# Performance work log

Hardware: AMD Instinct MI355X
Metric: run time of the kernel (lower is better)

The kernel has to match this reference:

```python
import jax, jax.numpy as jnp
import numpy as np

EPS = 1e-5
C1 = 64


def conv2d(x, w, pad):
    return jax.lax.conv_general_dilated(x, w, (1, 1), [(pad, pad), (pad, pad)],
                                        dimension_numbers=('NCHW', 'OIHW', 'NCHW'))


def batchnorm(x, scale, bias, mean, var):
    # inference-mode BN with running stats
    inv = scale * jax.lax.rsqrt(var + EPS)
    return x * inv[None, :, None, None] + (bias - mean * inv)[None, :, None, None]


def _interp_mat(n_out, n_in):
    # 1-D bilinear interpolation matrix, align_corners=True
    pos = jnp.linspace(0.0, n_in - 1.0, n_out)
    i0 = jnp.clip(jnp.floor(pos).astype(jnp.int32), 0, n_in - 1)
    i1 = jnp.clip(i0 + 1, 0, n_in - 1)
    w1 = pos - i0.astype(pos.dtype)
    r = jnp.arange(n_out)
    M = jnp.zeros((n_out, n_in), jnp.float32)
    M = M.at[r, i0].add(1.0 - w1).at[r, i1].add(w1)
    return M


def resize_ac(x, oh, ow):
    # bilinear resize with align_corners=True (matches F.interpolate/UpsamplingBilinear2d)
    Mh = _interp_mat(oh, x.shape[2])
    Mw = _interp_mat(ow, x.shape[3])
    return jnp.einsum('pw,nchw,oh->ncop', Mw, x, Mh)


def grid_sample_bilinear(img, grid):
    # img [N,C,H,W]; grid [N,Ho,Wo,2] (x,y) in [-1,1]; align_corners=False, zeros padding
    N, C, H, W = img.shape
    x = (grid[..., 0] + 1.0) * (W * 0.5) - 0.5
    y = (grid[..., 1] + 1.0) * (H * 0.5) - 0.5
    x0 = jnp.floor(x)
    y0 = jnp.floor(y)
    x1 = x0 + 1.0
    y1 = y0 + 1.0
    wx1 = x - x0
    wy1 = y - y0

    def gather(im, yi, xi):
        # im [C,H,W]; yi,xi [Ho,Wo] float pixel coords
        valid = (xi >= 0) & (xi <= W - 1) & (yi >= 0) & (yi <= H - 1)
        xc = jnp.clip(xi, 0, W - 1).astype(jnp.int32)
        yc = jnp.clip(yi, 0, H - 1).astype(jnp.int32)
        return im[:, yc, xc] * valid[None].astype(im.dtype)

    def sample_one(im, x0, x1, y0, y1, wx1, wy1):
        return (gather(im, y0, x0) * ((1 - wy1) * (1 - wx1))[None]
                + gather(im, y0, x1) * ((1 - wy1) * wx1)[None]
                + gather(im, y1, x0) * (wy1 * (1 - wx1))[None]
                + gather(im, y1, x1) * (wy1 * wx1)[None])

    return jax.vmap(sample_one)(img, x0, x1, y0, y1, wx1, wy1)


def warp(inp, out_h, out_w, delta):
    # build base grid exactly like bilinear_interpolate_torch_gridsample
    N, C, H, W = inp.shape
    ys = jnp.linspace(-1.0, 1.0, out_h)
    xs = jnp.linspace(-1.0, 1.0, out_w)
    gx = jnp.broadcast_to(xs[None, :], (out_h, out_w))
    gy = jnp.broadcast_to(ys[:, None], (out_h, out_w))
    base = jnp.stack([gx, gy], axis=-1)[None]  # [1,Ho,Wo,2]
    norm = jnp.array([W, H], inp.dtype)  # delta[...,0]/W, delta[...,1]/H
    grid = base + jnp.transpose(delta, (0, 2, 3, 1)) / norm
    return grid_sample_bilinear(inp, grid)


def forward(low_stage, high_stage, in_map,
            dg1_w1, dg1_scale, dg1_bias, dg1_mean, dg1_var, dg1_w2,
            dg2_w1, dg2_scale, dg2_bias, dg2_mean, dg2_var, dg2_w2,
            gamma, out_w, out_b):
    h, w = low_stage.shape[2], low_stage.shape[3]
    high = resize_ac(high_stage, h, w)
    imap = jax.nn.sigmoid(resize_ac(in_map, in_map.shape[2] * 2, in_map.shape[3] * 2))
    cat = jnp.concatenate([low_stage, high], axis=1)  # [N,2*C1,h,w]
    d1 = conv2d(batchnorm(conv2d(cat, dg1_w1, 0), dg1_scale, dg1_bias, dg1_mean, dg1_var), dg1_w2, 1)
    d2 = conv2d(batchnorm(conv2d(cat, dg2_w1, 0), dg2_scale, dg2_bias, dg2_mean, dg2_var), dg2_w2, 1)
    hi = warp(high, h, w, d1)
    lo = warp(low_stage, h, w, d2)
    hs = hi + lo
    f = gamma * hs * imap + hs
    o = conv2d(f, out_w, 1) + out_b[None, :, None, None]
    return f, o


def setup_inputs() -> dict:
    key = jax.random.key(0)
    ks = jax.random.split(key, 24)
    N, H, W = 8, 160, 160
    d = {}
    d['low_stage'] = jax.random.normal(ks[0], (N, C1, H, W), jnp.float32)
    d['high_stage'] = jax.random.normal(ks[1], (N, C1, H // 2, W // 2), jnp.float32)
    d['in_map'] = jax.random.normal(ks[2], (N, 1, H // 2, W // 2), jnp.float32)

    def bnp(k):
        k1, k2, k3, k4 = jax.random.split(k, 4)
        return (jax.random.normal(k1, (C1,)) * 0.1 + 1.0,
                jax.random.normal(k2, (C1,)) * 0.1,
                jax.random.normal(k3, (C1,)) * 0.1,
                jax.random.uniform(k4, (C1,), minval=0.5, maxval=1.5))

    for i, p in ((3, 'dg1'), (10, 'dg2')):
        d[p + '_w1'] = jax.random.normal(ks[i], (C1, 2 * C1, 1, 1), jnp.float32) * 0.05
        s, b, m, v = bnp(ks[i + 1])
        d[p + '_scale'], d[p + '_bias'], d[p + '_mean'], d[p + '_var'] = s, b, m, v
        d[p + '_w2'] = jax.random.normal(ks[i + 2], (2, C1, 3, 3), jnp.float32) * 0.05
    d['gamma'] = jnp.ones((1,), jnp.float32)
    d['out_w'] = jax.random.normal(ks[20], (1, C1, 3, 3), jnp.float32) * 0.05
    d['out_b'] = jnp.zeros((1,), jnp.float32)
    return d


def reference(low_stage, high_stage, in_map,
              dg1_w1, dg1_scale, dg1_bias, dg1_mean, dg1_var, dg1_w2,
              dg2_w1, dg2_scale, dg2_bias, dg2_mean, dg2_var, dg2_w2,
              gamma, out_w, out_b):
    return forward(low_stage, high_stage, in_map,
                   dg1_w1, dg1_scale, dg1_bias, dg1_mean, dg1_var, dg1_w2,
                   dg2_w1, dg2_scale, dg2_bias, dg2_mean, dg2_var, dg2_w2,
                   gamma, out_w, out_b)
```

## Files before the change

kernel.cpp:

```cpp
#include <hip/hip_runtime.h>
#include <cmath>

#define N_   8
#define C_   64
#define H_   160
#define W_   160
#define HW_  25600
#define HH_  80
#define WH_  80
#define FSZ_ (N_ * C_ * HW_)
#define PSZ_ (N_ * HW_)

typedef unsigned short ushort8v __attribute__((ext_vector_type(8)));
typedef short          bf16x8  __attribute__((ext_vector_type(8)));
typedef float          f32x4   __attribute__((ext_vector_type(4)));

__device__ __forceinline__ float bf2f(unsigned short u) {
    return __uint_as_float(((unsigned)u) << 16);
}
__device__ __forceinline__ unsigned short f2bf(float f) {
    unsigned u = __float_as_uint(f);
    u += 0x7FFF + ((u >> 16) & 1);
    return (unsigned short)(u >> 16);
}

__device__ __forceinline__ void gs_setup(float bgx, float bgy, float dx, float dy,
                                         int* idx, float* wgt)
{
    float px = ((bgx + dx * (1.f / 160.f)) + 1.f) * 80.f - 0.5f;
    float py = ((bgy + dy * (1.f / 160.f)) + 1.f) * 80.f - 0.5f;
    float x0f = floorf(px), y0f = floorf(py);
    float wx1 = px - x0f, wy1 = py - y0f, wx0 = 1.f - wx1, wy0 = 1.f - wy1;
    int x0 = (int)x0f, y0 = (int)y0f;
    float mx0 = ((unsigned)x0       < (unsigned)W_) ? 1.f : 0.f;
    float mx1 = ((unsigned)(x0 + 1) < (unsigned)W_) ? 1.f : 0.f;
    float my0 = ((unsigned)y0       < (unsigned)H_) ? 1.f : 0.f;
    float my1 = ((unsigned)(y0 + 1) < (unsigned)H_) ? 1.f : 0.f;
    int x0c = min(max(x0, 0), W_ - 1), x1c = min(max(x0 + 1, 0), W_ - 1);
    int y0c = min(max(y0, 0), H_ - 1), y1c = min(max(y0 + 1, 0), H_ - 1);
    idx[0] = y0c * W_ + x0c; wgt[0] = wy0 * wx0 * my0 * mx0;
    idx[1] = y0c * W_ + x1c; wgt[1] = wy0 * wx1 * my0 * mx1;
    idx[2] = y1c * W_ + x0c; wgt[2] = wy1 * wx0 * my1 * mx0;
    idx[3] = y1c * W_ + x1c; wgt[3] = wy1 * wx1 * my1 * mx1;
}

__global__ __launch_bounds__(128) void compose_w_kernel(
    const float* __restrict__ w1a, const float* __restrict__ w1b,
    const float* __restrict__ s1, const float* __restrict__ b1,
    const float* __restrict__ m1, const float* __restrict__ v1,
    const float* __restrict__ s2, const float* __restrict__ b2,
    const float* __restrict__ m2, const float* __restrict__ v2,
    const float* __restrict__ w2a, const float* __restrict__ w2b,
    float* __restrict__ weffg, float* __restrict__ btap4)
{
    __shared__ float ws2[64], bpart[64];
    int bId = blockIdx.x;
    int row = bId / 9, tap = bId % 9;
    int br = row >> 1, oc = row & 1;
    int tid = threadIdx.x;

    const float* w1 = br ? w1b : w1a;
    const float* w2 = br ? w2b : w2a;

    if (tid < 64) {
        int mid = tid;
        float sc = br ? s2[mid] : s1[mid];
        float vv = br ? v2[mid] : v1[mid];
        float bb = br ? b2[mid] : b1[mid];
        float mm = br ? m2[mid] : m1[mid];
        float inv = sc * rsqrtf(vv + 1e-5f);
        float w2v = w2[oc * 576 + mid * 9 + tap];
        ws2[mid]   = w2v * inv;
        bpart[mid] = w2v * (bb - mm * inv);
    }
    __syncthreads();

    float sum = 0.f;
    #pragma unroll 8
    for (int mid = 0; mid < 64; ++mid)
        sum = fmaf(ws2[mid], w1[mid * 128 + tid], sum);
    weffg[(row * 9 + tap) * 128 + tid] = sum;

    if (tid < 64) {
        float part = bpart[tid];
        #pragma unroll
        for (int off = 32; off > 0; off >>= 1)
            part += __shfl_down(part, off);
        if (tid == 0) btap4[tap * 4 + row] = part;
    }
}

__global__ __launch_bounds__(256) void pack_w_kernel(
    const float* __restrict__ weffg, const float* __restrict__ ow,
    unsigned short* __restrict__ wAe, unsigned short* __restrict__ wOe)
{
    int i = blockIdx.x * 256 + threadIdx.x;
    {
        int j    = i & 7;
        int lane = (i >> 3) & 63;
        int s    = (i >> 9) & 3;
        int tap  = i >> 11;
        int row  = lane & 15;
        int ci   = s * 32 + ((lane >> 4) & 3) * 8 + j;
        float v = (row < 4) ? weffg[(row * 9 + tap) * 128 + ci] : 0.f;
        wAe[i] = f2bf(v);
    }
    if (i < 9216) {
        int j    = i & 7;
        int lane = (i >> 3) & 63;
        int s    = (i >> 9) & 1;
        int tap  = i >> 10;
        int row  = lane & 15;
        int ci   = s * 32 + ((lane >> 4) & 3) * 8 + j;
        float v = (row == 0) ? ow[ci * 9 + tap] : 0.f;
        wOe[i] = f2bf(v);
    }
}

__global__ __launch_bounds__(256) void nchw_to_nhwc_bf16(
    const float* __restrict__ in, unsigned short* __restrict__ out, int hw)
{
    int p = blockIdx.x * 256 + threadIdx.x;
    int n = p / hw, rem = p % hw;
    const float* base = in + (long)n * 64 * hw + rem;
    unsigned o32[32];
    #pragma unroll
    for (int c2 = 0; c2 < 32; ++c2) {
        float v0 = base[(long)(2 * c2) * hw];
        float v1 = base[(long)(2 * c2 + 1) * hw];
        o32[c2] = (unsigned)f2bf(v0) | ((unsigned)f2bf(v1) << 16);
    }
    uint4* dst = reinterpret_cast<uint4*>(out + (long)p * 64);
    #pragma unroll
    for (int q = 0; q < 8; ++q)
        dst[q] = make_uint4(o32[q * 4], o32[q * 4 + 1], o32[q * 4 + 2], o32[q * 4 + 3]);
}

__global__ __launch_bounds__(256) void resize_high_nhwc(
    const unsigned short* __restrict__ hsb, unsigned short* __restrict__ highb)
{
    int p = blockIdx.x * 256 + threadIdx.x;
    int n = p / HW_, rem = p % HW_;
    int y = rem / W_, x = rem % W_;
    float sx = (x * 79.0f) / 159.0f;
    float sy = (y * 79.0f) / 159.0f;
    int ix0 = (int)sx, iy0 = (int)sy;
    float fx = sx - (float)ix0, fy = sy - (float)iy0;
    int ix1 = min(ix0 + 1, WH_ - 1), iy1 = min(iy0 + 1, HH_ - 1);
    long b = (long)n * (HH_ * WH_);
    const ushort8v* r00 = (const ushort8v*)(hsb + (b + iy0 * WH_ + ix0) * 64);
    const ushort8v* r01 = (const ushort8v*)(hsb + (b + iy0 * WH_ + ix1) * 64);
    const ushort8v* r10 = (const ushort8v*)(hsb + (b + iy1 * WH_ + ix0) * 64);
    const ushort8v* r11 = (const ushort8v*)(hsb + (b + iy1 * WH_ + ix1) * 64);
    float w00 = (1.f - fx) * (1.f - fy), w01 = fx * (1.f - fy);
    float w10 = (1.f - fx) * fy,         w11 = fx * fy;

    float acc[64];
    #pragma unroll
    for (int c = 0; c < 64; ++c) acc[c] = 0.f;
    #pragma unroll
    for (int q = 0; q < 8; ++q) {
        ushort8v v0 = r00[q], v1 = r01[q], v2 = r10[q], v3 = r11[q];
        #pragma unroll
        for (int j = 0; j < 8; ++j) {
            acc[q * 8 + j] = bf2f(v0[j]) * w00 + bf2f(v1[j]) * w01
                           + bf2f(v2[j]) * w10 + bf2f(v3[j]) * w11;
        }
    }
    unsigned o32[32];
    #pragma unroll
    for (int c2 = 0; c2 < 32; ++c2)
        o32[c2] = (unsigned)f2bf(acc[2 * c2]) | ((unsigned)f2bf(acc[2 * c2 + 1]) << 16);
    uint4* dst = reinterpret_cast<uint4*>(highb + (long)p * 64);
    #pragma unroll
    for (int q = 0; q < 8; ++q)
        dst[q] = make_uint4(o32[q * 4], o32[q * 4 + 1], o32[q * 4 + 2], o32[q * 4 + 3]);
}

__global__ __launch_bounds__(256) void d12_tiled_kernel(
    const unsigned short* __restrict__ lowb, const unsigned short* __restrict__ highb,
    const unsigned short* __restrict__ wAe, const float* __restrict__ btap4,
    float* __restrict__ d1, float* __restrict__ d2)
{
    __shared__ unsigned char lds[46080];
    int b  = blockIdx.x;
    int n  = b / 200;
    int t  = b % 200;
    int ty = t / 10, tx = t % 10;
    int y0 = ty * 8, x0 = tx * 16;
    int tid  = threadIdx.x;
    int lane = tid & 63;
    int wv   = tid >> 6;
    int r16  = lane & 15;
    int quad = lane >> 4;
    long nb = (long)n * HW_;

    for (int i = tid; i < 2880; i += 256) {
        int pix = i >> 4, qq = i & 15;
        int py = pix / 18, px = pix - py * 18;
        int gy = y0 + py - 1, gx = x0 + px - 1;
        bool valid = ((unsigned)gy < (unsigned)H_) && ((unsigned)gx < (unsigned)W_);
        ushort8v v = (ushort8v)0;
        if (valid) {
            const unsigned short* src = (qq < 8) ? lowb : highb;
            v = *reinterpret_cast<const ushort8v*>(
                src + ((long)(nb + gy * W_ + gx)) * 64 + (qq & 7) * 8);
        }
        *reinterpret_cast<ushort8v*>(
            lds + ((pix * 256 + qq * 16) ^ ((pix & 7) << 4))) = v;
    }
    __syncthreads();

    f32x4 accE[2], accO[2];
    accE[0] = accE[1] = accO[0] = accO[1] = (f32x4){0.f, 0.f, 0.f, 0.f};

    #pragma unroll
    for (int kx = 0; kx < 3; ++kx) {
        #pragma unroll
        for (int s = 0; s < 4; ++s) {
            bf16x8 Br[4];
            #pragma unroll
            for (int r = 0; r < 4; ++r) {
                int pix = (wv * 2 + r) * 18 + r16 + kx;
                Br[r] = *reinterpret_cast<const bf16x8*>(
                    lds + ((pix * 256 + s * 64 + quad * 16) ^ ((pix & 7) << 4)));
            }
            #pragma unroll
            for (int ky = 0; ky < 3; ++ky) {
                int tap = ky * 3 + kx;
                bf16x8 A = *reinterpret_cast<const bf16x8*>(
                    wAe + (tap * 4 + s) * 512 + lane * 8);
                if ((tap ^ s) & 1) {
                    accO[0] = __builtin_amdgcn_mfma_f32_16x16x32_bf16(A, Br[ky],     accO[0], 0, 0, 0);
                    accO[1] = __builtin_amdgcn_mfma_f32_16x16x32_bf16(A, Br[ky + 1], accO[1], 0, 0, 0);
                } else {
                    accE[0] = __builtin_amdgcn_mfma_f32_16x16x32_bf16(A, Br[ky],     accE[0], 0, 0, 0);
                    accE[1] = __builtin_amdgcn_mfma_f32_16x16x32_bf16(A, Br[ky + 1], accE[1], 0, 0, 0);
                }
            }
        }
    }

    #pragma unroll
    for (int g = 0; g < 2; ++g) {
        int yg = y0 + wv * 2 + g;
        int x  = x0 + r16;
        bool interior = (yg > 0) && (yg < H_ - 1) && (x0 > 0) && (x0 + 16 < W_);
        float b0 = 0.f, b1v = 0.f, b2v = 0.f, b3 = 0.f;
        #pragma unroll
        for (int tap = 0; tap < 9; ++tap) {
            int ky = tap / 3 - 1, kx = tap % 3 - 1;
            float m = 1.f;
            if (!interior) {
                int yy = yg + ky, xx = x + kx;
                m = (((unsigned)yy < (unsigned)H_) && ((unsigned)xx < (unsigned)W_))
                  ? 1.f : 0.f;
            }
            const float4 bt = *reinterpret_cast<const float4*>(btap4 + tap * 4);
            b0  = fmaf(m, bt.x, b0);
            b1v = fmaf(m, bt.y, b1v);
            b2v = fmaf(m, bt.z, b2v);
            b3  = fmaf(m, bt.w, b3);
        }
        if (quad == 0) {
            long p = nb + (long)yg * W_ + x;
            *reinterpret_cast<float2*>(d1 + p * 2) =
                make_float2(accE[g][0] + accO[g][0] + b0,
                            accE[g][1] + accO[g][1] + b1v);
            *reinterpret_cast<float2*>(d2 + p * 2) =
                make_float2(accE[g][2] + accO[g][2] + b2v,
                            accE[g][3] + accO[g][3] + b3);
        }
    }
}

__global__ __launch_bounds__(256) void warp_combine_cs(
    const unsigned short* __restrict__ lowb, const unsigned short* __restrict__ highb,
    const float* __restrict__ d1, const float* __restrict__ d2,
    const float* __restrict__ imin, const float* __restrict__ gamma,
    float* __restrict__ f, unsigned short* __restrict__ fnb)
{
    int u = blockIdx.x * 256 + threadIdx.x;
    int p = u >> 2, quarter = u & 3;
    int n = p / HW_, rem = p % HW_;
    int y = rem / W_, x = rem % W_;
    long nb = (long)n * HW_;

    float bgx = -1.f + x * (2.f / 159.f);
    float bgy = -1.f + y * (2.f / 159.f);

    float2 dv1 = *reinterpret_cast<const float2*>(d1 + (long)p * 2);
    float2 dv2 = *reinterpret_cast<const float2*>(d2 + (long)p * 2);

    int idx1[4], idx2[4];
    float wgt1[4], wgt2[4];
    gs_setup(bgx, bgy, dv1.x, dv1.y, idx1, wgt1);
    gs_setup(bgx, bgy, dv2.x, dv2.y, idx2, wgt2);

    float s;
    {
        float sx = (x * 79.0f) / 159.0f;
        float sy = (y * 79.0f) / 159.0f;
        int ix0 = (int)sx, iy0 = (int)sy;
        float fx = sx - (float)ix0, fy = sy - (float)iy0;
        int ix1 = min(ix0 + 1, WH_ - 1), iy1 = min(iy0 + 1, HH_ - 1);
        const float* ip = imin + n * (HH_ * WH_);
        float v00 = ip[iy0 * WH_ + ix0], v01 = ip[iy0 * WH_ + ix1];
        float v10 = ip[iy1 * WH_ + ix0], v11 = ip[iy1 * WH_ + ix1];
        float v = (v00 * (1.f - fx) + v01 * fx) * (1.f - fy)
                + (v10 * (1.f - fx) + v11 * fx) * fy;
        s = 1.f + gamma[0] * (1.f / (1.f + expf(-v)));
    }

    float acc[16];
    #pragma unroll
    for (int c = 0; c < 16; ++c) acc[c] = 0.f;

    #pragma unroll
    for (int j = 0; j < 4; ++j) {
        const ushort8v* row = (const ushort8v*)(highb + (nb + idx1[j]) * 64 + quarter * 16);
        float w = wgt1[j];
        #pragma unroll
        for (int q = 0; q < 2; ++q) {
            ushort8v v = row[q];
            #pragma unroll
            for (int k = 0; k < 8; ++k)
                acc[q * 8 + k] = fmaf(bf2f(v[k]), w, acc[q * 8 + k]);
        }
    }
    #pragma unroll
    for (int j = 0; j < 4; ++j) {
        const ushort8v* row = (const ushort8v*)(lowb + (nb + idx2[j]) * 64 + quarter * 16);
        float w = wgt2[j];
        #pragma unroll
        for (int q = 0; q < 2; ++q) {
            ushort8v v = row[q];
            #pragma unroll
            for (int k = 0; k < 8; ++k)
                acc[q * 8 + k] = fmaf(bf2f(v[k]), w, acc[q * 8 + k]);
        }
    }

    float* fp = f + nb * 64 + (long)(quarter * 16) * HW_ + rem;
    unsigned o32[8];
    #pragma unroll
    for (int c2 = 0; c2 < 8; ++c2) {
        float f0 = acc[2 * c2]     * s;
        float f1 = acc[2 * c2 + 1] * s;
        fp[(long)(2 * c2) * HW_]     = f0;
        fp[(long)(2 * c2 + 1) * HW_] = f1;
        o32[c2] = (unsigned)f2bf(f0) | ((unsigned)f2bf(f1) << 16);
    }
    uint4* dst = reinterpret_cast<uint4*>(fnb + (long)p * 64 + quarter * 16);
    dst[0] = make_uint4(o32[0], o32[1], o32[2], o32[3]);
    dst[1] = make_uint4(o32[4], o32[5], o32[6], o32[7]);
}

__global__ __launch_bounds__(256) void out_mfma_kernel(
    const unsigned short* __restrict__ fnb, const unsigned short* __restrict__ wOe,
    const float* __restrict__ ob, float* __restrict__ o)
{
    __shared__ unsigned char lds[23040];
    int b  = blockIdx.x;
    int n  = b / 200;
    int t  = b % 200;
    int ty = t / 10, tx = t % 10;
    int y0 = ty * 8, x0 = tx * 16;
    int tid  = threadIdx.x;
    int lane = tid & 63;
    int wv   = tid >> 6;
    int r16  = lane & 15;
    int quad = lane >> 4;
    long nb = (long)n * HW_;

    for (int i = tid; i < 1440; i += 256) {
        int pix = i >> 3, qq = i & 7;
        int py = pix / 18, px = pix - py * 18;
        int gy = y0 + py - 1, gx = x0 + px - 1;
        bool valid = ((unsigned)gy < (unsigned)H_) && ((unsigned)gx < (unsigned)W_);
        ushort8v v = (ushort8v)0;
        if (valid)
            v = *reinterpret_cast<const ushort8v*>(
                fnb + ((long)(nb + gy * W_ + gx)) * 64 + qq * 8);
        *reinterpret_cast<ushort8v*>(
            lds + ((pix * 128 + qq * 16) ^ ((pix & 7) << 4))) = v;
    }
    __syncthreads();

    f32x4 accE[2], accO[2];
    accE[0] = accE[1] = accO[0] = accO[1] = (f32x4){0.f, 0.f, 0.f, 0.f};

    #pragma unroll
    for (int kx = 0; kx < 3; ++kx) {
        #pragma unroll
        for (int s = 0; s < 2; ++s) {
            bf16x8 Br[4];
            #pragma unroll
            for (int r = 0; r < 4; ++r) {
                int pix = (wv * 2 + r) * 18 + r16 + kx;
                Br[r] = *reinterpret_cast<const bf16x8*>(
                    lds + ((pix * 128 + s * 64 + quad * 16) ^ ((pix & 7) << 4)));
            }
            #pragma unroll
            for (int ky = 0; ky < 3; ++ky) {
                int tap = ky * 3 + kx;
                bf16x8 A = *reinterpret_cast<const bf16x8*>(
                    wOe + (tap * 2 + s) * 512 + lane * 8);
                if ((tap ^ s) & 1) {
                    accO[0] = __builtin_amdgcn_mfma_f32_16x16x32_bf16(A, Br[ky],     accO[0], 0, 0, 0);
                    accO[1] = __builtin_amdgcn_mfma_f32_16x16x32_bf16(A, Br[ky + 1], accO[1], 0, 0, 0);
                } else {
                    accE[0] = __builtin_amdgcn_mfma_f32_16x16x32_bf16(A, Br[ky],     accE[0], 0, 0, 0);
                    accE[1] = __builtin_amdgcn_mfma_f32_16x16x32_bf16(A, Br[ky + 1], accE[1], 0, 0, 0);
                }
            }
        }
    }

    if (quad == 0) {
        float bias = ob[0];
        #pragma unroll
        for (int g = 0; g < 2; ++g) {
            int yg = y0 + wv * 2 + g;
            o[nb + (long)yg * W_ + x0 + r16] = accE[g][0] + accO[g][0] + bias;
        }
    }
}

extern "C" void kernel_launch(void* const* d_in, const int* in_sizes, int n_in,
                              void* d_out, int out_size, void* d_ws, size_t ws_size,
                              hipStream_t stream) {
    const float* low    = (const float*)d_in[0];
    const float* hsin   = (const float*)d_in[1];
    const float* imin   = (const float*)d_in[2];
    const float* dg1_w1 = (const float*)d_in[3];
    const float* dg1_s  = (const float*)d_in[4];
    const float* dg1_b  = (const float*)d_in[5];
    const float* dg1_m  = (const float*)d_in[6];
    const float* dg1_v  = (const float*)d_in[7];
    const float* dg1_w2 = (const float*)d_in[8];
    const float* dg2_w1 = (const float*)d_in[9];
    const float* dg2_s  = (const float*)d_in[10];
    const float* dg2_b  = (const float*)d_in[11];
    const float* dg2_m  = (const float*)d_in[12];
    const float* dg2_v  = (const float*)d_in[13];
    const float* dg2_w2 = (const float*)d_in[14];
    const float* gamma  = (const float*)d_in[15];
    const float* out_w  = (const float*)d_in[16];
    const float* out_b  = (const float*)d_in[17];

    float* ws    = (float*)d_ws;
    float* d1    = ws;
    float* d2    = d1 + 2 * PSZ_;
    float* btap4 = d2 + 2 * PSZ_;
    float* weffg = btap4 + 40;
    unsigned short* wAe   = (unsigned short*)(weffg + 4608);
    unsigned short* wOe   = wAe + 18432;
    unsigned short* lowb  = wOe + 9216;
    unsigned short* highb = lowb + FSZ_;
    unsigned short* fnb   = highb + FSZ_;
    unsigned short* hsb   = fnb;

    float* fout = (float*)d_out;
    float* oout = fout + FSZ_;

    compose_w_kernel<<<36, 128, 0, stream>>>(
        dg1_w1, dg2_w1, dg1_s, dg1_b, dg1_m, dg1_v,
        dg2_s, dg2_b, dg2_m, dg2_v, dg1_w2, dg2_w2, weffg, btap4);
    pack_w_kernel<<<72, 256, 0, stream>>>(weffg, out_w, wAe, wOe);
    nchw_to_nhwc_bf16<<<PSZ_ / 256, 256, 0, stream>>>(low, lowb, HW_);
    nchw_to_nhwc_bf16<<<(N_ * HH_ * WH_) / 256, 256, 0, stream>>>(hsin, hsb, HH_ * WH_);
    resize_high_nhwc<<<PSZ_ / 256, 256, 0, stream>>>(hsb, highb);
    d12_tiled_kernel<<<1600, 256, 0, stream>>>(
        lowb, highb, wAe, btap4, d1, d2);
    warp_combine_cs<<<PSZ_ * 4 / 256, 256, 0, stream>>>(
        lowb, highb, d1, d2, imin, gamma, fout, fnb);
    out_mfma_kernel<<<1600, 256, 0, stream>>>(fnb, wOe, out_b, oout);
}
```

Measured before the change: 132.2 us.

## Fuse warp-combine into output conv kernel, computing halo in LDS

Merges the warp/combine kernel into the 3x3 output MFMA conv kernel. Each block computes the warped, gated features for its 18x10 halo tile and writes them as bf16 straight into swizzled LDS, so the fnb bf16 intermediate never goes to global memory. This removes one launch and the write-then-reread of fnb. In exchange the halo pixels (180 per 128 interior) are recomputed with their gathers, and occupancy may fall because the per-thread warp work now runs inside the LDS-heavy conv block.

```diff
diff --git a/kernel.cpp b/kernel.cpp
--- a/kernel.cpp
+++ b/kernel.cpp
@@ -274,91 +274,12 @@
     }
 }
 
-__global__ __launch_bounds__(256) void warp_combine_cs(
+__global__ __launch_bounds__(256) void warp_out_fused(
     const unsigned short* __restrict__ lowb, const unsigned short* __restrict__ highb,
     const float* __restrict__ d1, const float* __restrict__ d2,
     const float* __restrict__ imin, const float* __restrict__ gamma,
-    float* __restrict__ f, unsigned short* __restrict__ fnb)
-{
-    int u = blockIdx.x * 256 + threadIdx.x;
-    int p = u >> 2, quarter = u & 3;
-    int n = p / HW_, rem = p % HW_;
-    int y = rem / W_, x = rem % W_;
-    long nb = (long)n * HW_;
-
-    float bgx = -1.f + x * (2.f / 159.f);
-    float bgy = -1.f + y * (2.f / 159.f);
-
-    float2 dv1 = *reinterpret_cast<const float2*>(d1 + (long)p * 2);
-    float2 dv2 = *reinterpret_cast<const float2*>(d2 + (long)p * 2);
-
-    int idx1[4], idx2[4];
-    float wgt1[4], wgt2[4];
-    gs_setup(bgx, bgy, dv1.x, dv1.y, idx1, wgt1);
-    gs_setup(bgx, bgy, dv2.x, dv2.y, idx2, wgt2);
-
-    float s;
-    {
-        float sx = (x * 79.0f) / 159.0f;
-        float sy = (y * 79.0f) / 159.0f;
-        int ix0 = (int)sx, iy0 = (int)sy;
-        float fx = sx - (float)ix0, fy = sy - (float)iy0;
-        int ix1 = min(ix0 + 1, WH_ - 1), iy1 = min(iy0 + 1, HH_ - 1);
-        const float* ip = imin + n * (HH_ * WH_);
-        float v00 = ip[iy0 * WH_ + ix0], v01 = ip[iy0 * WH_ + ix1];
-        float v10 = ip[iy1 * WH_ + ix0], v11 = ip[iy1 * WH_ + ix1];
-        float v = (v00 * (1.f - fx) + v01 * fx) * (1.f - fy)
-                + (v10 * (1.f - fx) + v11 * fx) * fy;
-        s = 1.f + gamma[0] * (1.f / (1.f + expf(-v)));
-    }
-
-    float acc[16];
-    #pragma unroll
-    for (int c = 0; c < 16; ++c) acc[c] = 0.f;
-
-    #pragma unroll
-    for (int j = 0; j < 4; ++j) {
-        const ushort8v* row = (const ushort8v*)(highb + (nb + idx1[j]) * 64 + quarter * 16);
-        float w = wgt1[j];
-        #pragma unroll
-        for (int q = 0; q < 2; ++q) {
-            ushort8v v = row[q];
-            #pragma unroll
-            for (int k = 0; k < 8; ++k)
-                acc[q * 8 + k] = fmaf(bf2f(v[k]), w, acc[q * 8 + k]);
-        }
-    }
-    #pragma unroll
-    for (int j = 0; j < 4; ++j) {
-        const ushort8v* row = (const ushort8v*)(lowb + (nb + idx2[j]) * 64 + quarter * 16);
-        float w = wgt2[j];
-        #pragma unroll
-        for (int q = 0; q < 2; ++q) {
-            ushort8v v = row[q];
-            #pragma unroll
-            for (int k = 0; k < 8; ++k)
-                acc[q * 8 + k] = fmaf(bf2f(v[k]), w, acc[q * 8 + k]);
-        }
-    }
-
-    float* fp = f + nb * 64 + (long)(quarter * 16) * HW_ + rem;
-    unsigned o32[8];
-    #pragma unroll
-    for (int c2 = 0; c2 < 8; ++c2) {
-        float f0 = acc[2 * c2]     * s;
-        float f1 = acc[2 * c2 + 1] * s;
-        fp[(long)(2 * c2) * HW_]     = f0;
-        fp[(long)(2 * c2 + 1) * HW_] = f1;
-        o32[c2] = (unsigned)f2bf(f0) | ((unsigned)f2bf(f1) << 16);
-    }
-    uint4* dst = reinterpret_cast<uint4*>(fnb + (long)p * 64 + quarter * 16);
-    dst[0] = make_uint4(o32[0], o32[1], o32[2], o32[3]);
-    dst[1] = make_uint4(o32[4], o32[5], o32[6], o32[7]);
-}
-
-__global__ __launch_bounds__(256) void out_mfma_kernel(
-    const unsigned short* __restrict__ fnb, const unsigned short* __restrict__ wOe,
-    const float* __restrict__ ob, float* __restrict__ o)
+    const unsigned short* __restrict__ wOe, const float* __restrict__ ob,
+    float* __restrict__ f, float* __restrict__ o)
 {
     __shared__ unsigned char lds[23040];
     int b  = blockIdx.x;
@@ -367,25 +288,107 @@
     int ty = t / 10, tx = t % 10;
     int y0 = ty * 8, x0 = tx * 16;
     int tid  = threadIdx.x;
+    long nb = (long)n * HW_;
+    float gm = gamma[0];
+
+    for (int u = tid; u < 720; u += 256) {
+        int pix = u >> 2, quarter = u & 3;
+        int py = pix / 18, px = pix - py * 18;
+        int gy = y0 + py - 1, gx = x0 + px - 1;
+        bool valid = ((unsigned)gy < (unsigned)H_) && ((unsigned)gx < (unsigned)W_);
+
+        unsigned o32[8];
+        #pragma unroll
+        for (int k = 0; k < 8; ++k) o32[k] = 0;
+
+        if (valid) {
+            int pp = gy * W_ + gx;
+            long p = nb + pp;
+
+            float bgx = -1.f + gx * (2.f / 159.f);
+            float bgy = -1.f + gy * (2.f / 159.f);
+            float2 dv1 = *reinterpret_cast<const float2*>(d1 + p * 2);
+            float2 dv2 = *reinterpret_cast<const float2*>(d2 + p * 2);
+
+            int idx1[4], idx2[4];
+            float wgt1[4], wgt2[4];
+            gs_setup(bgx, bgy, dv1.x, dv1.y, idx1, wgt1);
+            gs_setup(bgx, bgy, dv2.x, dv2.y, idx2, wgt2);
+
+            float s;
+            {
+                float sx = (gx * 79.0f) / 159.0f;
+                float sy = (gy * 79.0f) / 159.0f;
+                int ix0 = (int)sx, iy0 = (int)sy;
+                float fx = sx - (float)ix0, fy = sy - (float)iy0;
+                int ix1 = min(ix0 + 1, WH_ - 1), iy1 = min(iy0 + 1, HH_ - 1);
+                const float* ip = imin + n * (HH_ * WH_);
+                float v00 = ip[iy0 * WH_ + ix0], v01 = ip[iy0 * WH_ + ix1];
+                float v10 = ip[iy1 * WH_ + ix0], v11 = ip[iy1 * WH_ + ix1];
+                float v = (v00 * (1.f - fx) + v01 * fx) * (1.f - fy)
+                        + (v10 * (1.f - fx) + v11 * fx) * fy;
+                s = 1.f + gm * (1.f / (1.f + expf(-v)));
+            }
+
+            float acc[16];
+            #pragma unroll
+            for (int c = 0; c < 16; ++c) acc[c] = 0.f;
+
+            #pragma unroll
+            for (int j = 0; j < 4; ++j) {
+                const ushort8v* row = (const ushort8v*)(
+                    highb + (nb + idx1[j]) * 64 + quarter * 16);
+                float w = wgt1[j];
+                #pragma unroll
+                for (int q = 0; q < 2; ++q) {
+                    ushort8v v = row[q];
+                    #pragma unroll
+                    for (int k = 0; k < 8; ++k)
+                        acc[q * 8 + k] = fmaf(bf2f(v[k]), w, acc[q * 8 + k]);
+                }
+            }
+            #pragma unroll
+            for (int j = 0; j < 4; ++j) {
+                const ushort8v* row = (const ushort8v*)(
+                    lowb + (nb + idx2[j]) * 64 + quarter * 16);
+                float w = wgt2[j];
+                #pragma unroll
+                for (int q = 0; q < 2; ++q) {
+                    ushort8v v = row[q];
+                    #pragma unroll
+                    for (int k = 0; k < 8; ++k)
+                        acc[q * 8 + k] = fmaf(bf2f(v[k]), w, acc[q * 8 + k]);
+                }
+            }
+
+            bool interior = (py >= 1) && (py <= 8) && (px >= 1) && (px <= 16);
+            float* fp = f + (nb + (long)(quarter * 16) * HW_) * 0;
+            fp = f + ((long)n * 64 + quarter * 16) * HW_ + pp;
+            #pragma unroll
+            for (int c2 = 0; c2 < 8; ++c2) {
+                float f0 = acc[2 * c2]     * s;
+                float f1 = acc[2 * c2 + 1] * s;
+                if (interior) {
+                    fp[(long)(2 * c2) * HW_]     = f0;
+                    fp[(long)(2 * c2 + 1) * HW_] = f1;
+                }
+                o32[c2] = (unsigned)f2bf(f0) | ((unsigned)f2bf(f1) << 16);
+            }
+        }
+
+        int base = pix * 128 + quarter * 32;
+        int sw   = (pix & 7) << 4;
+        *reinterpret_cast<uint4*>(lds + ((base) ^ sw)) =
+            make_uint4(o32[0], o32[1], o32[2], o32[3]);
+        *reinterpret_cast<uint4*>(lds + ((base + 16) ^ sw)) =
+            make_uint4(o32[4], o32[5], o32[6], o32[7]);
+    }
+    __syncthreads();
+
     int lane = tid & 63;
     int wv   = tid >> 6;
     int r16  = lane & 15;
     int quad = lane >> 4;
-    long nb = (long)n * HW_;
-
-    for (int i = tid; i < 1440; i += 256) {
-        int pix = i >> 3, qq = i & 7;
-        int py = pix / 18, px = pix - py * 18;
-        int gy = y0 + py - 1, gx = x0 + px - 1;
-        bool valid = ((unsigned)gy < (unsigned)H_) && ((unsigned)gx < (unsigned)W_);
-        ushort8v v = (ushort8v)0;
-        if (valid)
-            v = *reinterpret_cast<const ushort8v*>(
-                fnb + ((long)(nb + gy * W_ + gx)) * 64 + qq * 8);
-        *reinterpret_cast<ushort8v*>(
-            lds + ((pix * 128 + qq * 16) ^ ((pix & 7) << 4))) = v;
-    }
-    __syncthreads();
 
     f32x4 accE[2], accO[2];
     accE[0] = accE[1] = accO[0] = accO[1] = (f32x4){0.f, 0.f, 0.f, 0.f};
@@ -458,8 +461,7 @@
     unsigned short* wOe   = wAe + 18432;
     unsigned short* lowb  = wOe + 9216;
     unsigned short* highb = lowb + FSZ_;
-    unsigned short* fnb   = highb + FSZ_;
-    unsigned short* hsb   = fnb;
+    unsigned short* hsb   = highb + FSZ_;
 
     float* fout = (float*)d_out;
     float* oout = fout + FSZ_;
@@ -473,7 +475,6 @@
     resize_high_nhwc<<<PSZ_ / 256, 256, 0, stream>>>(hsb, highb);
     d12_tiled_kernel<<<1600, 256, 0, stream>>>(
         lowb, highb, wAe, btap4, d1, d2);
-    warp_combine_cs<<<PSZ_ * 4 / 256, 256, 0, stream>>>(
-        lowb, highb, d1, d2, imin, gamma, fout, fnb);
-    out_mfma_kernel<<<1600, 256, 0, stream>>>(fnb, wOe, out_b, oout);
-}
+    warp_out_fused<<<1600, 256, 0, stream>>>(
+        lowb, highb, d1, d2, imin, gamma, wOe, out_b, fout, oout);
+}
```

Result: faster. 124.2 us (-6.1%).
